# Optimization experiments

Hardware: AMD Instinct MI355X
Metric: run time of the kernel (lower is better)

## Reference

```python
import math
import jax, jax.numpy as jnp
import numpy as np

HALF_PI = math.pi / 2
TWOR_SCALE = 1.0 / math.log(2.0)
B, C, L, K = 32, 2, 262144, 4


def setup_inputs() -> dict:
    key = jax.random.key(0)
    ks = jax.random.split(key, 6)
    return {
        "input_signal": jax.random.normal(ks[0], (B, C, L), jnp.float32),
        "twoR": jax.random.normal(ks[1], (B, K), jnp.float32),
        "G": jax.random.normal(ks[2], (B, K), jnp.float32),
        "c_hp": jax.random.normal(ks[3], (B, K), jnp.float32),
        "c_bp": jax.random.normal(ks[4], (B, K), jnp.float32),
        "c_lp": jax.random.normal(ks[5], (B, K), jnp.float32),
    }


def get_biquad_coefficients(twoR, G, c_hp, c_bp, c_lp):
    # each arg: (B, K)
    G2 = G * G
    b0 = c_hp + c_bp * G + c_lp * G2
    b1 = -2.0 * c_hp + 2.0 * c_lp * G2
    b2 = c_hp - c_bp * G + c_lp * G2
    a0 = 1.0 + G2 + twoR * G
    a1 = 2.0 * G2 - 2.0
    a2 = 1.0 + G2 - twoR * G
    return jnp.stack([b0, b1, b2], -1), jnp.stack([a0, a1, a2], -1)  # (B,K,3)


def _biquad_cascade(x, Bs, As):
    # x: (B,C,L); Bs, As: (B,1,K,3) -- broadcast over channels.
    # Direct-form II transposed, cascaded in series over K filters.
    Bs = Bs / As[..., :1]
    As = As / As[..., :1]
    b_, c_ = x.shape[0], x.shape[1]
    y = x
    num_filters = Bs.shape[2]
    for k in range(num_filters):
        b0, b1, b2 = Bs[:, :, k, 0], Bs[:, :, k, 1], Bs[:, :, k, 2]  # (B,1)
        a1, a2 = As[:, :, k, 1], As[:, :, k, 2]  # (B,1)

        def step(carry, xt):
            s1, s2 = carry
            yt = b0 * xt + s1              # (B,C)
            s1n = b1 * xt - a1 * yt + s2
            s2n = b2 * xt - a2 * yt
            return (s1n, s2n), yt

        init = (jnp.zeros((b_, c_), y.dtype), jnp.zeros((b_, c_), y.dtype))
        _, yT = jax.lax.scan(step, init, jnp.moveaxis(y, -1, 0))  # (L,B,C)
        y = jnp.moveaxis(yT, 0, -1)
    return y


def reference(input_signal, twoR, G, c_hp, c_bp, c_lp):
    G = jnp.tan(HALF_PI * jax.nn.sigmoid(G))
    twoR = TWOR_SCALE * jax.nn.softplus(twoR) + 0.01
    Bs, As = get_biquad_coefficients(twoR, G, c_hp, c_bp, c_lp)  # (B,K,3)
    Bs, As = Bs[:, None], As[:, None]  # unsqueeze(1): (B,1,K,3)
    return _biquad_cascade(input_signal, Bs, As)
```

## Files before the change

kernel.cpp:

```cpp
#include <hip/hip_runtime.h>
#include <math.h>

#define B_N 32
#define C_N 2
#define L_N 262144
#define K_N 4
#define NSEQ (B_N * C_N)
#define CHUNK 256
#define NCHUNK (L_N / CHUNK)
#define NLVL 10
#define WS_COEF 0
#define WS_MATS (B_N * K_N * 5)

__global__ __launch_bounds__(64) void svf_prep(
    const float* __restrict__ twoR, const float* __restrict__ Graw,
    const float* __restrict__ c_hp, const float* __restrict__ c_bp,
    const float* __restrict__ c_lp, float* __restrict__ ws)
{
    const int b = blockIdx.x;
    const int t = threadIdx.x;
    __shared__ double cf[K_N][5];
    __shared__ double M[8][8];

    if (t < K_N) {
        const int k = t;
        double g  = (double)Graw[b * K_N + k];
        double tr = (double)twoR[b * K_N + k];
        double hp = (double)c_hp[b * K_N + k];
        double bp = (double)c_bp[b * K_N + k];
        double lp = (double)c_lp[b * K_N + k];
        double sg = 1.0 / (1.0 + exp(-g));
        double G  = tan(1.5707963267948966 * sg);
        double R  = log1p(exp(tr)) * 1.4426950408889634 + 0.01;
        double G2 = G * G;
        double b0 = hp + bp * G + lp * G2;
        double b1 = -2.0 * hp + 2.0 * lp * G2;
        double b2 = hp - bp * G + lp * G2;
        double a0 = 1.0 + G2 + R * G;
        double a1 = 2.0 * G2 - 2.0;
        double a2 = 1.0 + G2 - R * G;
        cf[k][0] = b0 / a0; cf[k][1] = b1 / a0; cf[k][2] = b2 / a0;
        cf[k][3] = a1 / a0; cf[k][4] = a2 / a0;
    }
    __syncthreads();

    if (t < 20) ws[WS_COEF + b * 20 + t] = (float)cf[t / 5][t % 5];

    if (t < 8) {
        double s[8];
        #pragma unroll
        for (int i = 0; i < 8; ++i) s[i] = (i == t) ? 1.0 : 0.0;
        double in = 0.0;
        #pragma unroll
        for (int k = 0; k < K_N; ++k) {
            double y   = cf[k][0] * in + s[2 * k];
            double s1n = cf[k][1] * in - cf[k][3] * y + s[2 * k + 1];
            double s2n = cf[k][2] * in - cf[k][4] * y;
            s[2 * k] = s1n; s[2 * k + 1] = s2n; in = y;
        }
        #pragma unroll
        for (int i = 0; i < 8; ++i) M[i][t] = s[i];
    }
    __syncthreads();

    const int i = t >> 3, j = t & 7;
    for (int p = 1; p <= 17; ++p) {
        double acc = 0.0;
        #pragma unroll
        for (int k = 0; k < 8; ++k) acc += M[i][k] * M[k][j];
        __syncthreads();
        M[i][j] = acc;
        __syncthreads();
        if (p >= 8) ws[WS_MATS + (b * NLVL + (p - 8)) * 64 + t] = (float)acc;
    }
}

__device__ __forceinline__ float cascade_step(const float cf[20], float s[8], float in)
{
    #pragma unroll
    for (int k = 0; k < K_N; ++k) {
        float y  = fmaf(cf[k * 5 + 0], in, s[2 * k]);
        float t1 = fmaf(cf[k * 5 + 1], in, s[2 * k + 1]);
        float n1 = fmaf(-cf[k * 5 + 3], y, t1);
        float n2 = fmaf(-cf[k * 5 + 4], y, cf[k * 5 + 2] * in);
        s[2 * k] = n1; s[2 * k + 1] = n2;
        in = y;
    }
    return in;
}

__global__ __launch_bounds__(256) void svf_pass1(
    const float* __restrict__ x, const float* __restrict__ ws,
    float* __restrict__ out)
{
    const int g   = blockIdx.x * blockDim.x + threadIdx.x;
    const int seq = g >> 10;
    const int ci  = g & (NCHUNK - 1);
    const int b   = seq >> 1;
    float cf[20];
    #pragma unroll
    for (int q = 0; q < 20; ++q) cf[q] = ws[WS_COEF + b * 20 + q];

    const size_t base = (size_t)seq * L_N + (size_t)ci * CHUNK;
    const float4* xp = (const float4*)(x + base);
    float s[8] = {0, 0, 0, 0, 0, 0, 0, 0};

    for (int t4 = 0; t4 < CHUNK / 4; ++t4) {
        float4 v = xp[t4];
        (void)cascade_step(cf, s, v.x);
        (void)cascade_step(cf, s, v.y);
        (void)cascade_step(cf, s, v.z);
        (void)cascade_step(cf, s, v.w);
    }
    float4* fo = (float4*)(out + base + 8);
    fo[0] = make_float4(s[0], s[1], s[2], s[3]);
    fo[1] = make_float4(s[4], s[5], s[6], s[7]);
}

__global__ __launch_bounds__(1024) void svf_scan(
    const float* __restrict__ ws, float* __restrict__ out)
{
    const int seq = blockIdx.x;
    const int i   = threadIdx.x;
    const int b   = seq >> 1;
    __shared__ float Pm[NLVL][64];
    __shared__ float tb[NCHUNK][9];

    for (int q = threadIdx.x; q < NLVL * 64; q += blockDim.x)
        Pm[q >> 6][q & 63] = ws[WS_MATS + b * NLVL * 64 + q];

    const size_t base = (size_t)seq * L_N + (size_t)i * CHUNK;
    const float4* fp = (const float4*)(out + base + 8);
    float4 f0 = fp[0], f1 = fp[1];
    float t[8] = {f0.x, f0.y, f0.z, f0.w, f1.x, f1.y, f1.z, f1.w};
    __syncthreads();

    for (int l = 0; l < NLVL; ++l) {
        const int d = 1 << l;
        #pragma unroll
        for (int q = 0; q < 8; ++q) tb[i][q] = t[q];
        __syncthreads();
        float prev[8];
        const bool have = (i >= d);
        if (have) {
            #pragma unroll
            for (int q = 0; q < 8; ++q) prev[q] = tb[i - d][q];
        }
        __syncthreads();
        if (have) {
            #pragma unroll
            for (int r = 0; r < 8; ++r) {
                float acc = t[r];
                #pragma unroll
                for (int c = 0; c < 8; ++c)
                    acc = fmaf(Pm[l][r * 8 + c], prev[c], acc);
                t[r] = acc;
            }
        }
    }

    #pragma unroll
    for (int q = 0; q < 8; ++q) tb[i][q] = t[q];
    __syncthreads();
    float* so = out + base;
    if (i == 0) {
        #pragma unroll
        for (int q = 0; q < 8; ++q) so[q] = 0.0f;
    } else {
        #pragma unroll
        for (int q = 0; q < 8; ++q) so[q] = tb[i - 1][q];
    }
}

__global__ __launch_bounds__(256) void svf_pass2(
    const float* __restrict__ x, const float* __restrict__ ws,
    float* __restrict__ out)
{
    const int g   = blockIdx.x * blockDim.x + threadIdx.x;
    const int seq = g >> 10;
    const int ci  = g & (NCHUNK - 1);
    const int b   = seq >> 1;
    float cf[20];
    #pragma unroll
    for (int q = 0; q < 20; ++q) cf[q] = ws[WS_COEF + b * 20 + q];

    const size_t base = (size_t)seq * L_N + (size_t)ci * CHUNK;
    const float4* sp = (const float4*)(out + base);
    float4 s0 = sp[0], s1v = sp[1];
    float s[8] = {s0.x, s0.y, s0.z, s0.w, s1v.x, s1v.y, s1v.z, s1v.w};

    const float4* xp = (const float4*)(x + base);
    float4* yp = (float4*)(out + base);
    for (int t4 = 0; t4 < CHUNK / 4; ++t4) {
        float4 v = xp[t4];
        float y0 = cascade_step(cf, s, v.x);
        float y1 = cascade_step(cf, s, v.y);
        float y2 = cascade_step(cf, s, v.z);
        float y3 = cascade_step(cf, s, v.w);
        yp[t4] = make_float4(y0, y1, y2, y3);
    }
}

extern "C" void kernel_launch(void* const* d_in, const int* in_sizes, int n_in,
                              void* d_out, int out_size, void* d_ws, size_t ws_size,
                              hipStream_t stream)
{
    (void)in_sizes; (void)n_in; (void)out_size; (void)ws_size;
    const float* x    = (const float*)d_in[0];
    const float* twoR = (const float*)d_in[1];
    const float* G    = (const float*)d_in[2];
    const float* chp  = (const float*)d_in[3];
    const float* cbp  = (const float*)d_in[4];
    const float* clp  = (const float*)d_in[5];
    float* out = (float*)d_out;
    float* ws  = (float*)d_ws;

    svf_prep <<<B_N, 64, 0, stream>>>(twoR, G, chp, cbp, clp, ws);
    svf_pass1<<<NSEQ * NCHUNK / 256, 256, 0, stream>>>(x, ws, out);
    svf_scan <<<NSEQ, NCHUNK, 0, stream>>>(ws, out);
    svf_pass2<<<NSEQ * NCHUNK / 256, 256, 0, stream>>>(x, ws, out);
}
```

Measured before the change: 188.4 us.

## Shrink scan chunks and add per-thread serial group composition in scan

Chunk length drops from 256 to 32 samples, so the two sequential filter passes launch eight times as many threads, each with a much shorter dependent recurrence chain. The scan kernel keeps 1024 threads per sequence by having each thread serially combine 8 chunk states using a new 32-step transition matrix, which the prep kernel now stores. The scan then runs its log-step prefix across groups and expands the carry states back to every chunk. The cost is more state traffic between kernels and extra serial 8x8 matrix work in the scan.

```diff
diff --git a/kernel.cpp b/kernel.cpp
--- a/kernel.cpp
+++ b/kernel.cpp
@@ -6,11 +6,14 @@
 #define L_N 262144
 #define K_N 4
 #define NSEQ (B_N * C_N)
-#define CHUNK 256
+#define CHUNK 32
 #define NCHUNK (L_N / CHUNK)
+#define GRP 8
+#define NGRP (NCHUNK / GRP)
 #define NLVL 10
 #define WS_COEF 0
-#define WS_MATS (B_N * K_N * 5)
+#define WS_A32  (B_N * 20)
+#define WS_MATS (WS_A32 + B_N * 64)
 
 __global__ __launch_bounds__(64) void svf_prep(
     const float* __restrict__ twoR, const float* __restrict__ Graw,
@@ -71,6 +74,7 @@
         __syncthreads();
         M[i][j] = acc;
         __syncthreads();
+        if (p == 5) ws[WS_A32 + b * 64 + t] = (float)acc;
         if (p >= 8) ws[WS_MATS + (b * NLVL + (p - 8)) * 64 + t] = (float)acc;
     }
 }
@@ -94,7 +98,7 @@
     float* __restrict__ out)
 {
     const int g   = blockIdx.x * blockDim.x + threadIdx.x;
-    const int seq = g >> 10;
+    const int seq = g >> 13;
     const int ci  = g & (NCHUNK - 1);
     const int b   = seq >> 1;
     float cf[20];
@@ -105,6 +109,7 @@
     const float4* xp = (const float4*)(x + base);
     float s[8] = {0, 0, 0, 0, 0, 0, 0, 0};
 
+    #pragma unroll
     for (int t4 = 0; t4 < CHUNK / 4; ++t4) {
         float4 v = xp[t4];
         (void)cascade_step(cf, s, v.x);
@@ -124,16 +129,40 @@
     const int i   = threadIdx.x;
     const int b   = seq >> 1;
     __shared__ float Pm[NLVL][64];
-    __shared__ float tb[NCHUNK][9];
+    __shared__ float A32[64];
+    __shared__ float tb[NGRP][9];
 
     for (int q = threadIdx.x; q < NLVL * 64; q += blockDim.x)
         Pm[q >> 6][q & 63] = ws[WS_MATS + b * NLVL * 64 + q];
-
-    const size_t base = (size_t)seq * L_N + (size_t)i * CHUNK;
-    const float4* fp = (const float4*)(out + base + 8);
-    float4 f0 = fp[0], f1 = fp[1];
-    float t[8] = {f0.x, f0.y, f0.z, f0.w, f1.x, f1.y, f1.z, f1.w};
-    __syncthreads();
+    if (threadIdx.x < 64) A32[threadIdx.x] = ws[WS_A32 + b * 64 + threadIdx.x];
+
+    const size_t gbase = (size_t)seq * L_N + (size_t)i * (GRP * CHUNK);
+    float f[GRP][8];
+    #pragma unroll
+    for (int j = 0; j < GRP; ++j) {
+        const float4* fp = (const float4*)(out + gbase + (size_t)j * CHUNK + 8);
+        float4 a = fp[0], bv = fp[1];
+        f[j][0] = a.x; f[j][1] = a.y; f[j][2] = a.z; f[j][3] = a.w;
+        f[j][4] = bv.x; f[j][5] = bv.y; f[j][6] = bv.z; f[j][7] = bv.w;
+    }
+    __syncthreads();
+
+    float t[8];
+    #pragma unroll
+    for (int r = 0; r < 8; ++r) t[r] = f[0][r];
+    #pragma unroll
+    for (int j = 1; j < GRP; ++j) {
+        float nt[8];
+        #pragma unroll
+        for (int r = 0; r < 8; ++r) {
+            float acc = f[j][r];
+            #pragma unroll
+            for (int c = 0; c < 8; ++c) acc = fmaf(A32[r * 8 + c], t[c], acc);
+            nt[r] = acc;
+        }
+        #pragma unroll
+        for (int r = 0; r < 8; ++r) t[r] = nt[r];
+    }
 
     for (int l = 0; l < NLVL; ++l) {
         const int d = 1 << l;
@@ -162,13 +191,32 @@
     #pragma unroll
     for (int q = 0; q < 8; ++q) tb[i][q] = t[q];
     __syncthreads();
-    float* so = out + base;
+
+    float u[8];
     if (i == 0) {
         #pragma unroll
-        for (int q = 0; q < 8; ++q) so[q] = 0.0f;
+        for (int q = 0; q < 8; ++q) u[q] = 0.0f;
     } else {
         #pragma unroll
-        for (int q = 0; q < 8; ++q) so[q] = tb[i - 1][q];
+        for (int q = 0; q < 8; ++q) u[q] = tb[i - 1][q];
+    }
+    #pragma unroll
+    for (int j = 0; j < GRP; ++j) {
+        float4* so = (float4*)(out + gbase + (size_t)j * CHUNK);
+        so[0] = make_float4(u[0], u[1], u[2], u[3]);
+        so[1] = make_float4(u[4], u[5], u[6], u[7]);
+        if (j < GRP - 1) {
+            float nu[8];
+            #pragma unroll
+            for (int r = 0; r < 8; ++r) {
+                float acc = f[j][r];
+                #pragma unroll
+                for (int c = 0; c < 8; ++c) acc = fmaf(A32[r * 8 + c], u[c], acc);
+                nu[r] = acc;
+            }
+            #pragma unroll
+            for (int r = 0; r < 8; ++r) u[r] = nu[r];
+        }
     }
 }
 
@@ -177,7 +225,7 @@
     float* __restrict__ out)
 {
     const int g   = blockIdx.x * blockDim.x + threadIdx.x;
-    const int seq = g >> 10;
+    const int seq = g >> 13;
     const int ci  = g & (NCHUNK - 1);
     const int b   = seq >> 1;
     float cf[20];
@@ -191,6 +239,7 @@
 
     const float4* xp = (const float4*)(x + base);
     float4* yp = (float4*)(out + base);
+    #pragma unroll
     for (int t4 = 0; t4 < CHUNK / 4; ++t4) {
         float4 v = xp[t4];
         float y0 = cascade_step(cf, s, v.x);
@@ -217,6 +266,6 @@
 
     svf_prep <<<B_N, 64, 0, stream>>>(twoR, G, chp, cbp, clp, ws);
     svf_pass1<<<NSEQ * NCHUNK / 256, 256, 0, stream>>>(x, ws, out);
-    svf_scan <<<NSEQ, NCHUNK, 0, stream>>>(ws, out);
+    svf_scan <<<NSEQ, NCHUNK / GRP, 0, stream>>>(ws, out);
     svf_pass2<<<NSEQ * NCHUNK / 256, 256, 0, stream>>>(x, ws, out);
 }
```

New measurement: 268.2 us. +42.3%, slower.

## Restructure chunked biquad scan into hierarchical block scan with smaller chunks

Applied to the files above, without the earlier changes.

Chunk size drops from 256 to 64 samples, so each sequence splits into more chunks and there is more parallelism. The intra-block prefix scan of chunk end-states moves into pass1, and a tiny serial kernel scans the per-block aggregates. Pass2 rebuilds each thread's carry-in by applying matrix powers to the block prefix using the bits of the thread id. This trades the 1024-thread single-block scan for extra per-thread matrix work in pass2 and a serial 16-step scan per sequence.

```diff
diff --git a/kernel.cpp b/kernel.cpp
--- a/kernel.cpp
+++ b/kernel.cpp
@@ -6,11 +6,18 @@
 #define L_N 262144
 #define K_N 4
 #define NSEQ (B_N * C_N)
-#define CHUNK 256
-#define NCHUNK (L_N / CHUNK)
-#define NLVL 10
+#define CHUNK 64
+#define THREADS 256
+#define BLKSAMP (CHUNK * THREADS)
+#define NBLK_SEQ (L_N / BLKSAMP)
+#define NBLK_TOT (NSEQ * NBLK_SEQ)
+#define NLVL 8
+
 #define WS_COEF 0
-#define WS_MATS (B_N * K_N * 5)
+#define WS_PL   (B_N * 20)
+#define WS_PBLK (WS_PL + B_N * 8 * 64)
+#define WS_AGG  (WS_PBLK + B_N * 64)
+#define WS_SBLK (WS_AGG + NBLK_TOT * 8)
 
 __global__ __launch_bounds__(64) void svf_prep(
     const float* __restrict__ twoR, const float* __restrict__ Graw,
@@ -64,14 +71,15 @@
     __syncthreads();
 
     const int i = t >> 3, j = t & 7;
-    for (int p = 1; p <= 17; ++p) {
+    for (int p = 1; p <= 14; ++p) {
         double acc = 0.0;
         #pragma unroll
         for (int k = 0; k < 8; ++k) acc += M[i][k] * M[k][j];
         __syncthreads();
         M[i][j] = acc;
         __syncthreads();
-        if (p >= 8) ws[WS_MATS + (b * NLVL + (p - 8)) * 64 + t] = (float)acc;
+        if (p >= 6 && p <= 13) ws[WS_PL + (b * 8 + (p - 6)) * 64 + t] = (float)acc;
+        if (p == 14)           ws[WS_PBLK + b * 64 + t] = (float)acc;
     }
 }
 
@@ -89,62 +97,48 @@
     return in;
 }
 
-__global__ __launch_bounds__(256) void svf_pass1(
+__global__ __launch_bounds__(THREADS) void svf_pass1(
     const float* __restrict__ x, const float* __restrict__ ws,
     float* __restrict__ out)
 {
-    const int g   = blockIdx.x * blockDim.x + threadIdx.x;
-    const int seq = g >> 10;
-    const int ci  = g & (NCHUNK - 1);
+    const int seq = blockIdx.x >> 4;
+    const int blk = blockIdx.x & (NBLK_SEQ - 1);
+    const int tid = threadIdx.x;
     const int b   = seq >> 1;
+
+    __shared__ float Pm[NLVL][64];
+    __shared__ float tb[THREADS][9];
+
+    for (int q = tid; q < NLVL * 64; q += THREADS)
+        Pm[q >> 6][q & 63] = ws[WS_PL + b * 8 * 64 + q];
+
     float cf[20];
     #pragma unroll
     for (int q = 0; q < 20; ++q) cf[q] = ws[WS_COEF + b * 20 + q];
 
-    const size_t base = (size_t)seq * L_N + (size_t)ci * CHUNK;
+    const size_t base = (size_t)seq * L_N + (size_t)blk * BLKSAMP + (size_t)tid * CHUNK;
     const float4* xp = (const float4*)(x + base);
-    float s[8] = {0, 0, 0, 0, 0, 0, 0, 0};
-
+    float t[8] = {0, 0, 0, 0, 0, 0, 0, 0};
+    #pragma unroll
     for (int t4 = 0; t4 < CHUNK / 4; ++t4) {
         float4 v = xp[t4];
-        (void)cascade_step(cf, s, v.x);
-        (void)cascade_step(cf, s, v.y);
-        (void)cascade_step(cf, s, v.z);
-        (void)cascade_step(cf, s, v.w);
-    }
-    float4* fo = (float4*)(out + base + 8);
-    fo[0] = make_float4(s[0], s[1], s[2], s[3]);
-    fo[1] = make_float4(s[4], s[5], s[6], s[7]);
-}
-
-__global__ __launch_bounds__(1024) void svf_scan(
-    const float* __restrict__ ws, float* __restrict__ out)
-{
-    const int seq = blockIdx.x;
-    const int i   = threadIdx.x;
-    const int b   = seq >> 1;
-    __shared__ float Pm[NLVL][64];
-    __shared__ float tb[NCHUNK][9];
-
-    for (int q = threadIdx.x; q < NLVL * 64; q += blockDim.x)
-        Pm[q >> 6][q & 63] = ws[WS_MATS + b * NLVL * 64 + q];
-
-    const size_t base = (size_t)seq * L_N + (size_t)i * CHUNK;
-    const float4* fp = (const float4*)(out + base + 8);
-    float4 f0 = fp[0], f1 = fp[1];
-    float t[8] = {f0.x, f0.y, f0.z, f0.w, f1.x, f1.y, f1.z, f1.w};
+        (void)cascade_step(cf, t, v.x);
+        (void)cascade_step(cf, t, v.y);
+        (void)cascade_step(cf, t, v.z);
+        (void)cascade_step(cf, t, v.w);
+    }
     __syncthreads();
 
     for (int l = 0; l < NLVL; ++l) {
         const int d = 1 << l;
         #pragma unroll
-        for (int q = 0; q < 8; ++q) tb[i][q] = t[q];
+        for (int q = 0; q < 8; ++q) tb[tid][q] = t[q];
         __syncthreads();
         float prev[8];
-        const bool have = (i >= d);
+        const bool have = (tid >= d);
         if (have) {
             #pragma unroll
-            for (int q = 0; q < 8; ++q) prev[q] = tb[i - d][q];
+            for (int q = 0; q < 8; ++q) prev[q] = tb[tid - d][q];
         }
         __syncthreads();
         if (have) {
@@ -160,43 +154,120 @@
     }
 
     #pragma unroll
-    for (int q = 0; q < 8; ++q) tb[i][q] = t[q];
-    __syncthreads();
-    float* so = out + base;
-    if (i == 0) {
-        #pragma unroll
-        for (int q = 0; q < 8; ++q) so[q] = 0.0f;
+    for (int q = 0; q < 8; ++q) tb[tid][q] = t[q];
+    __syncthreads();
+
+    float e[8];
+    if (tid == 0) {
+        #pragma unroll
+        for (int q = 0; q < 8; ++q) e[q] = 0.0f;
     } else {
         #pragma unroll
-        for (int q = 0; q < 8; ++q) so[q] = tb[i - 1][q];
-    }
-}
-
-__global__ __launch_bounds__(256) void svf_pass2(
+        for (int q = 0; q < 8; ++q) e[q] = tb[tid - 1][q];
+    }
+    float4* eo = (float4*)(out + base);
+    eo[0] = make_float4(e[0], e[1], e[2], e[3]);
+    eo[1] = make_float4(e[4], e[5], e[6], e[7]);
+
+    if (tid == THREADS - 1) {
+        float* agg = (float*)ws + WS_AGG + (size_t)blockIdx.x * 8;
+        #pragma unroll
+        for (int q = 0; q < 8; ++q) agg[q] = t[q];
+    }
+}
+
+__global__ __launch_bounds__(64) void svf_scanb(float* __restrict__ ws)
+{
+    const int seq = threadIdx.x;
+    const int b   = seq >> 1;
+    float P[64];
+    #pragma unroll
+    for (int q = 0; q < 64; ++q) P[q] = ws[WS_PBLK + b * 64 + q];
+
+    const float* agg = ws + WS_AGG + (size_t)seq * NBLK_SEQ * 8;
+    float* sb        = ws + WS_SBLK + (size_t)seq * NBLK_SEQ * 8;
+
+    float t[8] = {0, 0, 0, 0, 0, 0, 0, 0};
+    float f[8];
+    #pragma unroll
+    for (int q = 0; q < 8; ++q) f[q] = agg[q];
+
+    for (int j = 0; j < NBLK_SEQ; ++j) {
+        float fn[8];
+        if (j + 1 < NBLK_SEQ) {
+            #pragma unroll
+            for (int q = 0; q < 8; ++q) fn[q] = agg[(j + 1) * 8 + q];
+        }
+        #pragma unroll
+        for (int q = 0; q < 8; ++q) sb[j * 8 + q] = t[q];
+        float nt[8];
+        #pragma unroll
+        for (int r = 0; r < 8; ++r) {
+            float acc = f[r];
+            #pragma unroll
+            for (int c = 0; c < 8; ++c) acc = fmaf(P[r * 8 + c], t[c], acc);
+            nt[r] = acc;
+        }
+        #pragma unroll
+        for (int q = 0; q < 8; ++q) { t[q] = nt[q]; f[q] = fn[q]; }
+    }
+}
+
+__global__ __launch_bounds__(THREADS) void svf_pass2(
     const float* __restrict__ x, const float* __restrict__ ws,
     float* __restrict__ out)
 {
-    const int g   = blockIdx.x * blockDim.x + threadIdx.x;
-    const int seq = g >> 10;
-    const int ci  = g & (NCHUNK - 1);
+    const int seq = blockIdx.x >> 4;
+    const int blk = blockIdx.x & (NBLK_SEQ - 1);
+    const int tid = threadIdx.x;
     const int b   = seq >> 1;
+
+    __shared__ float Pm[NLVL][64];
+    for (int q = tid; q < NLVL * 64; q += THREADS)
+        Pm[q >> 6][q & 63] = ws[WS_PL + b * 8 * 64 + q];
+
     float cf[20];
     #pragma unroll
     for (int q = 0; q < 20; ++q) cf[q] = ws[WS_COEF + b * 20 + q];
 
-    const size_t base = (size_t)seq * L_N + (size_t)ci * CHUNK;
+    const float* sbp = ws + WS_SBLK + (size_t)blockIdx.x * 8;
+    float v[8];
+    #pragma unroll
+    for (int q = 0; q < 8; ++q) v[q] = sbp[q];
+    __syncthreads();
+
+    #pragma unroll
+    for (int l = 0; l < NLVL; ++l) {
+        if ((tid >> l) & 1) {
+            float nv[8];
+            #pragma unroll
+            for (int r = 0; r < 8; ++r) {
+                float acc = 0.0f;
+                #pragma unroll
+                for (int c = 0; c < 8; ++c)
+                    acc = fmaf(Pm[l][r * 8 + c], v[c], acc);
+                nv[r] = acc;
+            }
+            #pragma unroll
+            for (int q = 0; q < 8; ++q) v[q] = nv[q];
+        }
+    }
+
+    const size_t base = (size_t)seq * L_N + (size_t)blk * BLKSAMP + (size_t)tid * CHUNK;
     const float4* sp = (const float4*)(out + base);
-    float4 s0 = sp[0], s1v = sp[1];
-    float s[8] = {s0.x, s0.y, s0.z, s0.w, s1v.x, s1v.y, s1v.z, s1v.w};
+    float4 e0 = sp[0], e1 = sp[1];
+    float s[8] = {e0.x + v[0], e0.y + v[1], e0.z + v[2], e0.w + v[3],
+                  e1.x + v[4], e1.y + v[5], e1.z + v[6], e1.w + v[7]};
 
     const float4* xp = (const float4*)(x + base);
     float4* yp = (float4*)(out + base);
+    #pragma unroll
     for (int t4 = 0; t4 < CHUNK / 4; ++t4) {
-        float4 v = xp[t4];
-        float y0 = cascade_step(cf, s, v.x);
-        float y1 = cascade_step(cf, s, v.y);
-        float y2 = cascade_step(cf, s, v.z);
-        float y3 = cascade_step(cf, s, v.w);
+        float4 xv = xp[t4];
+        float y0 = cascade_step(cf, s, xv.x);
+        float y1 = cascade_step(cf, s, xv.y);
+        float y2 = cascade_step(cf, s, xv.z);
+        float y3 = cascade_step(cf, s, xv.w);
         yp[t4] = make_float4(y0, y1, y2, y3);
     }
 }
@@ -216,7 +287,7 @@
     float* ws  = (float*)d_ws;
 
     svf_prep <<<B_N, 64, 0, stream>>>(twoR, G, chp, cbp, clp, ws);
-    svf_pass1<<<NSEQ * NCHUNK / 256, 256, 0, stream>>>(x, ws, out);
-    svf_scan <<<NSEQ, NCHUNK, 0, stream>>>(ws, out);
-    svf_pass2<<<NSEQ * NCHUNK / 256, 256, 0, stream>>>(x, ws, out);
-}
+    svf_pass1<<<NBLK_TOT, THREADS, 0, stream>>>(x, ws, out);
+    svf_scanb<<<1, 64, 0, stream>>>(ws);
+    svf_pass2<<<NBLK_TOT, THREADS, 0, stream>>>(x, ws, out);
+}
```

Measured after the change: 202.0 us. +7.2%, slower.
